# Kernel optimization log

Measured on AMD Instinct MI355X. Metric: run time of the kernel, lower is better.

The kernel has to match this reference:

```python
import jax, jax.numpy as jnp
import numpy as np

N_NODES = 10000
N_EDGES = 640000
D_FEAT = 128


def setup_inputs() -> dict:
    key = jax.random.key(0)
    k1, k2, k3 = jax.random.split(key, 3)
    feat = jax.random.normal(k1, (N_NODES, D_FEAT), dtype=jnp.float32)
    src = jax.random.randint(k2, (N_EDGES,), 0, N_NODES, dtype=jnp.int64)
    dst = jax.random.randint(k3, (N_EDGES,), 0, N_NODES, dtype=jnp.int64)
    beta = jnp.ones((1,), dtype=jnp.float32)
    return {"feat": feat, "src": src, "dst": dst, "beta": beta}


def reference(feat, src, dst, beta):
    # L2-normalize node features along feature dim (eps matches torch F.normalize)
    norm = feat / jnp.maximum(jnp.linalg.norm(feat, axis=-1, keepdims=True), 1e-12)
    # per-edge cosine similarity: sum over d of norm[src] * norm[dst]  -> [E]
    cos = jnp.einsum('ed,ed->e', norm[src], norm[dst])
    e = beta[0] * cos
    # edge softmax segmented over destination nodes
    seg_max = jax.ops.segment_max(e, dst, num_segments=N_NODES)  # [N]
    ex = jnp.exp(e - seg_max[dst])                               # [E]
    seg_sum = jax.ops.segment_sum(ex, dst, num_segments=N_NODES)  # [N]
    p = ex / seg_sum[dst]                                        # [E]
    # weighted neighbor aggregation: sum_e p_e * feat[src_e] into dst
    msg = feat[src] * p[:, None]                                 # [E, d]
    out = jax.ops.segment_sum(msg, dst, num_segments=N_NODES)    # [N, d]
    return out
```

## Files before the change

kernel.cpp:

```cpp
#include <hip/hip_runtime.h>
#include <math.h>

#define D_FEAT 128
#define NB_HIST 128
#define N_NODES_MAX 10016
#define CAP 192

__device__ __forceinline__ unsigned short f2bf(float x) {
    unsigned int b = __float_as_uint(x);
    return (unsigned short)((b + 0x7fffu + ((b >> 16) & 1u)) >> 16);
}
__device__ __forceinline__ float2 bf2_to_f2(unsigned int u) {
    return make_float2(__uint_as_float(u << 16), __uint_as_float(u & 0xffff0000u));
}

__global__ __launch_bounds__(1024) void hist_norm_kernel(
        const float* __restrict__ feat,
        const int* __restrict__ dst,
        unsigned int* __restrict__ nfb,
        float* __restrict__ invn,
        int* __restrict__ hist,
        unsigned short* __restrict__ lrank,
        int n_nodes, int n_edges, int epb) {
    __shared__ int lhist[N_NODES_MAX];
    int tid = (int)threadIdx.x;
    if ((int)blockIdx.x < NB_HIST) {
        int b = blockIdx.x;
        for (int i = tid; i < n_nodes; i += 1024) lhist[i] = 0;
        __syncthreads();
        int e0 = b * epb;
        int e1 = e0 + epb;
        if (e1 > n_edges) e1 = n_edges;
        for (int e = e0 + tid; e < e1; e += 1024) {
            int d = dst[e];
            lrank[e] = (unsigned short)atomicAdd(&lhist[d], 1);
        }
        __syncthreads();
        for (int i = tid; i < n_nodes; i += 1024)
            hist[b * n_nodes + i] = lhist[i];
    } else {
        int node = ((int)blockIdx.x - NB_HIST) * 16 + (tid >> 6);
        int lane = tid & 63;
        if (node >= n_nodes) return;
        float2 f = ((const float2*)feat)[node * 64 + lane];
        float ss = f.x * f.x + f.y * f.y;
        #pragma unroll
        for (int off = 1; off < 64; off <<= 1)
            ss += __shfl_xor(ss, off, 64);
        unsigned int lo = f2bf(f.x), hi = f2bf(f.y);
        nfb[node * 64 + lane] = (hi << 16) | lo;
        if (lane == 0) invn[node] = 1.0f / fmaxf(sqrtf(ss), 1e-12f);
    }
}

__global__ __launch_bounds__(256) void scan_kernel(int* __restrict__ hist,
                                                   int* __restrict__ cnt,
                                                   int n_nodes) {
    int node = (int)(blockIdx.x * blockDim.x + threadIdx.x);
    if (node >= n_nodes) return;
    int base = 0;
    #pragma unroll 8
    for (int b = 0; b < NB_HIST; ++b) {
        int idx = b * n_nodes + node;
        int v = hist[idx];
        hist[idx] = base;
        base += v;
    }
    cnt[node] = base;
}

__global__ __launch_bounds__(256) void scatter_kernel(
        const int* __restrict__ src,
        const int* __restrict__ dst,
        const int* __restrict__ hist,
        const unsigned short* __restrict__ lrank,
        unsigned short* __restrict__ src_sorted,
        int n_nodes, int n_edges, int epb) {
    int e = blockIdx.x * blockDim.x + threadIdx.x;
    if (e >= n_edges) return;
    int d = dst[e];
    int b = e / epb;
    int r = hist[b * n_nodes + d] + (int)lrank[e];
    if (r < CAP)
        src_sorted[(size_t)d * CAP + r] = (unsigned short)src[e];
}

__global__ void agg_kernel(const unsigned int* __restrict__ nfb,
                           const float* __restrict__ invn,
                           const float* __restrict__ beta,
                           const int* __restrict__ cnt,
                           const unsigned short* __restrict__ src_sorted,
                           float* __restrict__ out, int n_nodes) {
    int node = (int)(blockIdx.x * blockDim.x + threadIdx.x) >> 6;
    int lane = threadIdx.x & 63;
    if (node >= n_nodes) return;
    int deg = cnt[node];
    if (deg > CAP) deg = CAP;
    int beg = node * CAP;
    int end = beg + deg;
    int q  = lane >> 4;
    int ql = lane & 15;
    float bd = beta[0] * invn[node];

    uint4 du = ((const uint4*)nfb)[(size_t)node * 16 + ql];
    float2 d0 = bf2_to_f2(du.x), d1 = bf2_to_f2(du.y);
    float2 d2 = bf2_to_f2(du.z), d3 = bf2_to_f2(du.w);

    float l = 0.0f;
    float a0 = 0.f, a1 = 0.f, a2 = 0.f, a3 = 0.f;
    float a4 = 0.f, a5 = 0.f, a6 = 0.f, a7 = 0.f;

    for (int base = beg; base < end; base += 64) {
        int nb = end - base;
        if (nb > 64) nb = 64;
        int gi = base + lane;
        bool valid = gi < end;
        int idx = valid ? (int)src_sorted[gi] : 0;
        float ivm = valid ? invn[idx] : 0.0f;

        #pragma unroll 8
        for (int j = 0; j < nb; j += 4) {
            int jj = j + q;
            int   sj  = __shfl(idx, jj, 64);
            float inj = __shfl(ivm, jj, 64);
            uint4 u = ((const uint4*)nfb)[(size_t)sj * 16 + ql];
            float2 f0 = bf2_to_f2(u.x), f1 = bf2_to_f2(u.y);
            float2 f2 = bf2_to_f2(u.z), f3 = bf2_to_f2(u.w);
            float part = f0.x * d0.x + f0.y * d0.y + f1.x * d1.x + f1.y * d1.y
                       + f2.x * d2.x + f2.y * d2.y + f3.x * d3.x + f3.y * d3.y;
            part += __shfl_xor(part, 1, 64);
            part += __shfl_xor(part, 2, 64);
            part += __shfl_xor(part, 4, 64);
            part += __shfl_xor(part, 8, 64);
            float w = __expf(part * inj * bd);
            w = (inj > 0.0f) ? w : 0.0f;
            l += w;
            a0 += w * f0.x;  a1 += w * f0.y;
            a2 += w * f1.x;  a3 += w * f1.y;
            a4 += w * f2.x;  a5 += w * f2.y;
            a6 += w * f3.x;  a7 += w * f3.y;
        }
    }
    #pragma unroll
    for (int off = 1; off < 64; off <<= 1)
        l += __shfl_xor(l, off, 64);
    a0 += __shfl_xor(a0, 16, 64); a0 += __shfl_xor(a0, 32, 64);
    a1 += __shfl_xor(a1, 16, 64); a1 += __shfl_xor(a1, 32, 64);
    a2 += __shfl_xor(a2, 16, 64); a2 += __shfl_xor(a2, 32, 64);
    a3 += __shfl_xor(a3, 16, 64); a3 += __shfl_xor(a3, 32, 64);
    a4 += __shfl_xor(a4, 16, 64); a4 += __shfl_xor(a4, 32, 64);
    a5 += __shfl_xor(a5, 16, 64); a5 += __shfl_xor(a5, 32, 64);
    a6 += __shfl_xor(a6, 16, 64); a6 += __shfl_xor(a6, 32, 64);
    a7 += __shfl_xor(a7, 16, 64); a7 += __shfl_xor(a7, 32, 64);
    float invl = (l > 0.0f) ? (16.0f / l) : 0.0f;
    if (q == 0) {
        float4* o = (float4*)out + (size_t)node * 32 + ql * 2;
        o[0] = make_float4(a0 * invl, a1 * invl, a2 * invl, a3 * invl);
        o[1] = make_float4(a4 * invl, a5 * invl, a6 * invl, a7 * invl);
    }
}

extern "C" void kernel_launch(void* const* d_in, const int* in_sizes, int n_in,
                              void* d_out, int out_size, void* d_ws, size_t ws_size,
                              hipStream_t stream) {
    const float* feat = (const float*)d_in[0];
    const int* src    = (const int*)d_in[1];
    const int* dst    = (const int*)d_in[2];
    const float* beta = (const float*)d_in[3];
    float* out = (float*)d_out;

    const int n_nodes = in_sizes[0] / D_FEAT;
    const int n_edges = in_sizes[1];
    const int epb = (n_edges + NB_HIST - 1) / NB_HIST;

    char* ws = (char*)d_ws;
    size_t off = 0;
    auto alloc = [&](size_t bytes) -> void* {
        void* p = ws + off;
        off += (bytes + 255) & ~(size_t)255;
        return p;
    };
    unsigned int*   nfb        = (unsigned int*)alloc((size_t)n_nodes * 64 * 4);
    float*          invn       = (float*)alloc((size_t)n_nodes * 4);
    int*            hist       = (int*)  alloc((size_t)NB_HIST * n_nodes * 4);
    int*            cnt        = (int*)  alloc((size_t)n_nodes * 4);
    unsigned short* lrank      = (unsigned short*)alloc((size_t)n_edges * 2);
    unsigned short* src_sorted = (unsigned short*)alloc((size_t)n_nodes * CAP * 2);

    int nb_norm = (n_nodes + 15) / 16;
    hist_norm_kernel<<<NB_HIST + nb_norm, 1024, 0, stream>>>(
        feat, dst, nfb, invn, hist, lrank, n_nodes, n_edges, epb);

    scan_kernel<<<(n_nodes + 255) / 256, 256, 0, stream>>>(hist, cnt, n_nodes);

    scatter_kernel<<<(n_edges + 255) / 256, 256, 0, stream>>>(
        src, dst, hist, lrank, src_sorted, n_nodes, n_edges, epb);

    agg_kernel<<<(n_nodes + 3) / 4, 256, 0, stream>>>(
        nfb, invn, beta, cnt, src_sorted, out, n_nodes);
}
```

Measured before the change: 122.0 us.

## Fuse four kernels into one persistent kernel with software grid barriers

Merges the histogram/normalize, scan, scatter and aggregation kernels into a single persistent kernel of 256 blocks × 1024 threads, separating the phases with atomic-counter grid barriers. The barrier counters are zeroed by a memset before launch. This removes three kernel launch gaps and inter-kernel drain. It risks lower occupancy in the aggregation phase, since 40KB of LDS per block and 1024 threads limit residency. It could also deadlock if not all 256 blocks are co-resident. The scan phase uses only 40 threads per block.

```diff
diff --git a/kernel.cpp b/kernel.cpp
--- a/kernel.cpp
+++ b/kernel.cpp
@@ -3,8 +3,11 @@
 
 #define D_FEAT 128
 #define NB_HIST 128
+#define NBLOCKS 256
+#define NTHREADS 1024
 #define N_NODES_MAX 10016
 #define CAP 192
+
 
 __device__ __forceinline__ unsigned short f2bf(float x) {
     unsigned int b = __float_as_uint(x);
@@ -14,149 +17,156 @@
     return make_float2(__uint_as_float(u << 16), __uint_as_float(u & 0xffff0000u));
 }
 
-__global__ __launch_bounds__(1024) void hist_norm_kernel(
+__device__ __forceinline__ void grid_barrier(unsigned int* bar) {
+    __syncthreads();
+    if (threadIdx.x == 0) {
+        __threadfence();
+        __hip_atomic_fetch_add(bar, 1u, __ATOMIC_RELAXED, __HIP_MEMORY_SCOPE_AGENT);
+        while (__hip_atomic_load(bar, __ATOMIC_RELAXED, __HIP_MEMORY_SCOPE_AGENT)
+               < (unsigned)NBLOCKS)
+            __builtin_amdgcn_s_sleep(1);
+        __threadfence();
+    }
+    __syncthreads();
+}
+
+__global__ __launch_bounds__(NTHREADS) void mega_kernel(
         const float* __restrict__ feat,
+        const int* __restrict__ src,
         const int* __restrict__ dst,
+        const float* __restrict__ beta,
         unsigned int* __restrict__ nfb,
         float* __restrict__ invn,
         int* __restrict__ hist,
         unsigned short* __restrict__ lrank,
+        unsigned short* __restrict__ src_sorted,
+        int* __restrict__ cnt,
+        unsigned int* __restrict__ bars,
+        float* __restrict__ out,
         int n_nodes, int n_edges, int epb) {
     __shared__ int lhist[N_NODES_MAX];
-    int tid = (int)threadIdx.x;
-    if ((int)blockIdx.x < NB_HIST) {
-        int b = blockIdx.x;
-        for (int i = tid; i < n_nodes; i += 1024) lhist[i] = 0;
+    const int tid = (int)threadIdx.x;
+    const int bid = (int)blockIdx.x;
+    const int lane = tid & 63;
+
+    if (bid < NB_HIST) {
+        for (int i = tid; i < n_nodes; i += NTHREADS) lhist[i] = 0;
         __syncthreads();
-        int e0 = b * epb;
-        int e1 = e0 + epb;
-        if (e1 > n_edges) e1 = n_edges;
-        for (int e = e0 + tid; e < e1; e += 1024) {
+        int e0 = bid * epb;
+        int e1 = e0 + epb; if (e1 > n_edges) e1 = n_edges;
+        for (int e = e0 + tid; e < e1; e += NTHREADS) {
             int d = dst[e];
             lrank[e] = (unsigned short)atomicAdd(&lhist[d], 1);
         }
         __syncthreads();
-        for (int i = tid; i < n_nodes; i += 1024)
-            hist[b * n_nodes + i] = lhist[i];
+        for (int i = tid; i < n_nodes; i += NTHREADS)
+            hist[bid * n_nodes + i] = lhist[i];
     } else {
-        int node = ((int)blockIdx.x - NB_HIST) * 16 + (tid >> 6);
-        int lane = tid & 63;
-        if (node >= n_nodes) return;
-        float2 f = ((const float2*)feat)[node * 64 + lane];
-        float ss = f.x * f.x + f.y * f.y;
+        for (int node = (bid - NB_HIST) * 16 + (tid >> 6); node < n_nodes;
+             node += (NBLOCKS - NB_HIST) * 16) {
+            float2 f = ((const float2*)feat)[node * 64 + lane];
+            float ss = f.x * f.x + f.y * f.y;
+            #pragma unroll
+            for (int off = 1; off < 64; off <<= 1)
+                ss += __shfl_xor(ss, off, 64);
+            unsigned int lo = f2bf(f.x), hi = f2bf(f.y);
+            nfb[node * 64 + lane] = (hi << 16) | lo;
+            if (lane == 0) invn[node] = 1.0f / fmaxf(sqrtf(ss), 1e-12f);
+        }
+    }
+    grid_barrier(&bars[0]);
+
+    {
+        int node = bid * 40 + tid;
+        if (tid < 40 && node < n_nodes) {
+            int base = 0;
+            #pragma unroll 8
+            for (int b = 0; b < NB_HIST; ++b) {
+                int idx = b * n_nodes + node;
+                int v = hist[idx];
+                hist[idx] = base;
+                base += v;
+            }
+            cnt[node] = base;
+        }
+    }
+    grid_barrier(&bars[32]);
+
+    for (int e = bid * NTHREADS + tid; e < n_edges; e += NBLOCKS * NTHREADS) {
+        int d = dst[e];
+        int b = e / epb;
+        int r = hist[b * n_nodes + d] + (int)lrank[e];
+        if (r < CAP)
+            src_sorted[(size_t)d * CAP + r] = (unsigned short)src[e];
+    }
+    grid_barrier(&bars[64]);
+
+    const int q  = lane >> 4;
+    const int ql = lane & 15;
+    const float beta0 = beta[0];
+    for (int node = bid * 16 + (tid >> 6); node < n_nodes; node += NBLOCKS * 16) {
+        int deg = cnt[node];
+        if (deg > CAP) deg = CAP;
+        int beg = node * CAP;
+        int end = beg + deg;
+        float bd = beta0 * invn[node];
+
+        uint4 du = ((const uint4*)nfb)[(size_t)node * 16 + ql];
+        float2 d0 = bf2_to_f2(du.x), d1 = bf2_to_f2(du.y);
+        float2 d2 = bf2_to_f2(du.z), d3 = bf2_to_f2(du.w);
+
+        float l = 0.0f;
+        float a0 = 0.f, a1 = 0.f, a2 = 0.f, a3 = 0.f;
+        float a4 = 0.f, a5 = 0.f, a6 = 0.f, a7 = 0.f;
+
+        for (int base = beg; base < end; base += 64) {
+            int nb = end - base;
+            if (nb > 64) nb = 64;
+            int gi = base + lane;
+            bool valid = gi < end;
+            int idx = valid ? (int)src_sorted[gi] : 0;
+            float ivm = valid ? invn[idx] : 0.0f;
+
+            #pragma unroll 8
+            for (int j = 0; j < nb; j += 4) {
+                int jj = j + q;
+                int   sj  = __shfl(idx, jj, 64);
+                float inj = __shfl(ivm, jj, 64);
+                uint4 u = ((const uint4*)nfb)[(size_t)sj * 16 + ql];
+                float2 f0 = bf2_to_f2(u.x), f1 = bf2_to_f2(u.y);
+                float2 f2 = bf2_to_f2(u.z), f3 = bf2_to_f2(u.w);
+                float part = f0.x * d0.x + f0.y * d0.y + f1.x * d1.x + f1.y * d1.y
+                           + f2.x * d2.x + f2.y * d2.y + f3.x * d3.x + f3.y * d3.y;
+                part += __shfl_xor(part, 1, 64);
+                part += __shfl_xor(part, 2, 64);
+                part += __shfl_xor(part, 4, 64);
+                part += __shfl_xor(part, 8, 64);
+                float w = __expf(part * inj * bd);
+                w = (inj > 0.0f) ? w : 0.0f;
+                l += w;
+                a0 += w * f0.x;  a1 += w * f0.y;
+                a2 += w * f1.x;  a3 += w * f1.y;
+                a4 += w * f2.x;  a5 += w * f2.y;
+                a6 += w * f3.x;  a7 += w * f3.y;
+            }
+        }
         #pragma unroll
         for (int off = 1; off < 64; off <<= 1)
-            ss += __shfl_xor(ss, off, 64);
-        unsigned int lo = f2bf(f.x), hi = f2bf(f.y);
-        nfb[node * 64 + lane] = (hi << 16) | lo;
-        if (lane == 0) invn[node] = 1.0f / fmaxf(sqrtf(ss), 1e-12f);
-    }
-}
-
-__global__ __launch_bounds__(256) void scan_kernel(int* __restrict__ hist,
-                                                   int* __restrict__ cnt,
-                                                   int n_nodes) {
-    int node = (int)(blockIdx.x * blockDim.x + threadIdx.x);
-    if (node >= n_nodes) return;
-    int base = 0;
-    #pragma unroll 8
-    for (int b = 0; b < NB_HIST; ++b) {
-        int idx = b * n_nodes + node;
-        int v = hist[idx];
-        hist[idx] = base;
-        base += v;
-    }
-    cnt[node] = base;
-}
-
-__global__ __launch_bounds__(256) void scatter_kernel(
-        const int* __restrict__ src,
-        const int* __restrict__ dst,
-        const int* __restrict__ hist,
-        const unsigned short* __restrict__ lrank,
-        unsigned short* __restrict__ src_sorted,
-        int n_nodes, int n_edges, int epb) {
-    int e = blockIdx.x * blockDim.x + threadIdx.x;
-    if (e >= n_edges) return;
-    int d = dst[e];
-    int b = e / epb;
-    int r = hist[b * n_nodes + d] + (int)lrank[e];
-    if (r < CAP)
-        src_sorted[(size_t)d * CAP + r] = (unsigned short)src[e];
-}
-
-__global__ void agg_kernel(const unsigned int* __restrict__ nfb,
-                           const float* __restrict__ invn,
-                           const float* __restrict__ beta,
-                           const int* __restrict__ cnt,
-                           const unsigned short* __restrict__ src_sorted,
-                           float* __restrict__ out, int n_nodes) {
-    int node = (int)(blockIdx.x * blockDim.x + threadIdx.x) >> 6;
-    int lane = threadIdx.x & 63;
-    if (node >= n_nodes) return;
-    int deg = cnt[node];
-    if (deg > CAP) deg = CAP;
-    int beg = node * CAP;
-    int end = beg + deg;
-    int q  = lane >> 4;
-    int ql = lane & 15;
-    float bd = beta[0] * invn[node];
-
-    uint4 du = ((const uint4*)nfb)[(size_t)node * 16 + ql];
-    float2 d0 = bf2_to_f2(du.x), d1 = bf2_to_f2(du.y);
-    float2 d2 = bf2_to_f2(du.z), d3 = bf2_to_f2(du.w);
-
-    float l = 0.0f;
-    float a0 = 0.f, a1 = 0.f, a2 = 0.f, a3 = 0.f;
-    float a4 = 0.f, a5 = 0.f, a6 = 0.f, a7 = 0.f;
-
-    for (int base = beg; base < end; base += 64) {
-        int nb = end - base;
-        if (nb > 64) nb = 64;
-        int gi = base + lane;
-        bool valid = gi < end;
-        int idx = valid ? (int)src_sorted[gi] : 0;
-        float ivm = valid ? invn[idx] : 0.0f;
-
-        #pragma unroll 8
-        for (int j = 0; j < nb; j += 4) {
-            int jj = j + q;
-            int   sj  = __shfl(idx, jj, 64);
-            float inj = __shfl(ivm, jj, 64);
-            uint4 u = ((const uint4*)nfb)[(size_t)sj * 16 + ql];
-            float2 f0 = bf2_to_f2(u.x), f1 = bf2_to_f2(u.y);
-            float2 f2 = bf2_to_f2(u.z), f3 = bf2_to_f2(u.w);
-            float part = f0.x * d0.x + f0.y * d0.y + f1.x * d1.x + f1.y * d1.y
-                       + f2.x * d2.x + f2.y * d2.y + f3.x * d3.x + f3.y * d3.y;
-            part += __shfl_xor(part, 1, 64);
-            part += __shfl_xor(part, 2, 64);
-            part += __shfl_xor(part, 4, 64);
-            part += __shfl_xor(part, 8, 64);
-            float w = __expf(part * inj * bd);
-            w = (inj > 0.0f) ? w : 0.0f;
-            l += w;
-            a0 += w * f0.x;  a1 += w * f0.y;
-            a2 += w * f1.x;  a3 += w * f1.y;
-            a4 += w * f2.x;  a5 += w * f2.y;
-            a6 += w * f3.x;  a7 += w * f3.y;
-        }
-    }
-    #pragma unroll
-    for (int off = 1; off < 64; off <<= 1)
-        l += __shfl_xor(l, off, 64);
-    a0 += __shfl_xor(a0, 16, 64); a0 += __shfl_xor(a0, 32, 64);
-    a1 += __shfl_xor(a1, 16, 64); a1 += __shfl_xor(a1, 32, 64);
-    a2 += __shfl_xor(a2, 16, 64); a2 += __shfl_xor(a2, 32, 64);
-    a3 += __shfl_xor(a3, 16, 64); a3 += __shfl_xor(a3, 32, 64);
-    a4 += __shfl_xor(a4, 16, 64); a4 += __shfl_xor(a4, 32, 64);
-    a5 += __shfl_xor(a5, 16, 64); a5 += __shfl_xor(a5, 32, 64);
-    a6 += __shfl_xor(a6, 16, 64); a6 += __shfl_xor(a6, 32, 64);
-    a7 += __shfl_xor(a7, 16, 64); a7 += __shfl_xor(a7, 32, 64);
-    float invl = (l > 0.0f) ? (16.0f / l) : 0.0f;
-    if (q == 0) {
-        float4* o = (float4*)out + (size_t)node * 32 + ql * 2;
-        o[0] = make_float4(a0 * invl, a1 * invl, a2 * invl, a3 * invl);
-        o[1] = make_float4(a4 * invl, a5 * invl, a6 * invl, a7 * invl);
+            l += __shfl_xor(l, off, 64);
+        a0 += __shfl_xor(a0, 16, 64); a0 += __shfl_xor(a0, 32, 64);
+        a1 += __shfl_xor(a1, 16, 64); a1 += __shfl_xor(a1, 32, 64);
+        a2 += __shfl_xor(a2, 16, 64); a2 += __shfl_xor(a2, 32, 64);
+        a3 += __shfl_xor(a3, 16, 64); a3 += __shfl_xor(a3, 32, 64);
+        a4 += __shfl_xor(a4, 16, 64); a4 += __shfl_xor(a4, 32, 64);
+        a5 += __shfl_xor(a5, 16, 64); a5 += __shfl_xor(a5, 32, 64);
+        a6 += __shfl_xor(a6, 16, 64); a6 += __shfl_xor(a6, 32, 64);
+        a7 += __shfl_xor(a7, 16, 64); a7 += __shfl_xor(a7, 32, 64);
+        float invl = (l > 0.0f) ? (16.0f / l) : 0.0f;
+        if (q == 0) {
+            float4* o = (float4*)out + (size_t)node * 32 + ql * 2;
+            o[0] = make_float4(a0 * invl, a1 * invl, a2 * invl, a3 * invl);
+            o[1] = make_float4(a4 * invl, a5 * invl, a6 * invl, a7 * invl);
+        }
     }
 }
 
@@ -186,16 +196,11 @@
     int*            cnt        = (int*)  alloc((size_t)n_nodes * 4);
     unsigned short* lrank      = (unsigned short*)alloc((size_t)n_edges * 2);
     unsigned short* src_sorted = (unsigned short*)alloc((size_t)n_nodes * CAP * 2);
-
-    int nb_norm = (n_nodes + 15) / 16;
-    hist_norm_kernel<<<NB_HIST + nb_norm, 1024, 0, stream>>>(
-        feat, dst, nfb, invn, hist, lrank, n_nodes, n_edges, epb);
-
-    scan_kernel<<<(n_nodes + 255) / 256, 256, 0, stream>>>(hist, cnt, n_nodes);
-
-    scatter_kernel<<<(n_edges + 255) / 256, 256, 0, stream>>>(
-        src, dst, hist, lrank, src_sorted, n_nodes, n_edges, epb);
-
-    agg_kernel<<<(n_nodes + 3) / 4, 256, 0, stream>>>(
-        nfb, invn, beta, cnt, src_sorted, out, n_nodes);
-}
+    unsigned int*   bars       = (unsigned int*)alloc(512);
+
+    hipMemsetAsync(bars, 0, 512, stream);
+
+    mega_kernel<<<NBLOCKS, NTHREADS, 0, stream>>>(
+        feat, src, dst, beta, nfb, invn, hist, lrank, src_sorted, cnt, bars,
+        out, n_nodes, n_edges, epb);
+}
```

Measured after the change: 203.6 us. +66.8%, slower.
